# Kernel optimization log

Measured on AMD Instinct MI355X. Metric: run time of the kernel, lower is better.

## Reference

```python
import jax, jax.numpy as jnp
import numpy as np

INPUT_DIM = 80
ENC_DIM = 256
ATTN_DIM = 128
GRU_DIM = 256
B = 32
T_ENC = 800
T_DEC = 400


def setup_inputs() -> dict:
    key = jax.random.key(0)
    ks = jax.random.split(key, 12)
    s = 0.05
    d = {}
    d['enc_feat'] = jax.random.normal(ks[0], (B, T_ENC, ENC_DIM), jnp.float32)
    d['ground_truth'] = jax.random.normal(ks[1], (B, T_DEC, INPUT_DIM), jnp.float32)
    # GRU (PyTorch layout): weight_ih (3*G, in), weight_hh (3*G, G)
    d['W_ih'] = jax.random.normal(ks[2], (3 * GRU_DIM, INPUT_DIM + ENC_DIM), jnp.float32) * s
    d['W_hh'] = jax.random.normal(ks[3], (3 * GRU_DIM, GRU_DIM), jnp.float32) * s
    d['b_ih'] = jax.random.normal(ks[4], (3 * GRU_DIM,), jnp.float32) * s
    d['b_hh'] = jax.random.normal(ks[5], (3 * GRU_DIM,), jnp.float32) * s
    # Additive attention: v^T tanh(W_enc e + W_dec h + b)
    d['W_enc'] = jax.random.normal(ks[6], (ATTN_DIM, ENC_DIM), jnp.float32) * s
    d['W_dec'] = jax.random.normal(ks[7], (ATTN_DIM, GRU_DIM), jnp.float32) * s
    d['b_attn'] = jax.random.normal(ks[8], (ATTN_DIM,), jnp.float32) * s
    d['v_attn'] = jax.random.normal(ks[9], (ATTN_DIM,), jnp.float32) * s
    # output_trans: Linear(gru_dim + enc_feat_dim -> input_dim)
    d['W_out'] = jax.random.normal(ks[10], (INPUT_DIM, GRU_DIM + ENC_DIM), jnp.float32) * s
    d['b_out'] = jax.random.normal(ks[11], (INPUT_DIM,), jnp.float32) * s
    return d


def reference(enc_feat, ground_truth, W_ih, W_hh, b_ih, b_hh,
              W_enc, W_dec, b_attn, v_attn, W_out, b_out):
    # Teacher-forced decode (teacher_force_rate=1.0): max_step = T_dec,
    # input at each step is ground_truth[:, t, :].
    Bsz, T_enc, E = enc_feat.shape
    G = W_hh.shape[1]
    # Encoder projection for additive attention (step-invariant)
    enc_proj = jnp.einsum('bte,ae->bta', enc_feat, W_enc)  # (B, T_enc, attn_dim)

    def step(carry, x_t):
        h, ctx = carry  # h: (B,G), ctx: (B,E)
        inp = jnp.concatenate([x_t, ctx], axis=-1)  # (B, input_dim+E)
        gi = inp @ W_ih.T + b_ih
        gh = h @ W_hh.T + b_hh
        ir, iz, inn = jnp.split(gi, 3, axis=-1)
        hr, hz, hn = jnp.split(gh, 3, axis=-1)
        r = jax.nn.sigmoid(ir + hr)
        z = jax.nn.sigmoid(iz + hz)
        n = jnp.tanh(inn + r * hn)
        h_new = (1.0 - z) * n + z * h  # PyTorch GRU update
        # additive attention over encoder timesteps
        dec_proj = h_new @ W_dec.T + b_attn  # (B, attn_dim)
        scores = jnp.einsum('bta,a->bt', jnp.tanh(enc_proj + dec_proj[:, None, :]), v_attn)
        attn = jax.nn.softmax(scores, axis=-1)  # (B, T_enc)
        ctx_new = jnp.einsum('bt,bte->be', attn, enc_feat)  # (B, E)
        concat = jnp.concatenate([h_new, ctx_new], axis=-1)
        pred = jax.nn.log_softmax(concat @ W_out.T + b_out, axis=-1)
        return (h_new, ctx_new), (pred, attn)

    h0 = jnp.zeros((Bsz, G), enc_feat.dtype)
    c0 = jnp.zeros((Bsz, E), enc_feat.dtype)
    xs = jnp.swapaxes(ground_truth, 0, 1)  # (T_dec, B, input_dim)
    _, (preds, attns) = jax.lax.scan(step, (h0, c0), xs)
    pred_seq = jnp.swapaxes(preds, 0, 1)    # (B, T_dec, input_dim)
    attn_record = jnp.swapaxes(attns, 0, 1)  # (B, T_dec, T_enc)
    return pred_seq, attn_record
```

## Files before the change

### kernel.cpp

```cpp
#include <hip/hip_runtime.h>

#define BB    32
#define TDEC  400
#define TENC  800
#define EDIM  256
#define GDIM  256
#define ADIM  128
#define IDIM  80
#define G3    768
#define NSL   8
#define SLH   32
#define SLT   100
#define XCST  257
#define EPST  136
#define ETST  102

typedef unsigned short u16;
typedef unsigned int u32;
typedef unsigned long long u64;

__device__ __forceinline__ float b2f(u16 u) {
  union { u32 i; float f; } x; x.i = ((u32)u) << 16; return x.f;
}
__device__ __forceinline__ u16 f2b(float f) {
  union { float f; u32 u; } x; x.f = f;
  u32 u = x.u; u += 0x7fffu + ((u >> 16) & 1u);
  return (u16)(u >> 16);
}
__device__ __forceinline__ void ld8(const u16* p, float* w) {
  const uint4 q = *reinterpret_cast<const uint4*>(p);
  union { u32 i; float f; } c;
  c.i = q.x << 16;          w[0] = c.f;
  c.i = q.x & 0xffff0000u;  w[1] = c.f;
  c.i = q.y << 16;          w[2] = c.f;
  c.i = q.y & 0xffff0000u;  w[3] = c.f;
  c.i = q.z << 16;          w[4] = c.f;
  c.i = q.z & 0xffff0000u;  w[5] = c.f;
  c.i = q.w << 16;          w[6] = c.f;
  c.i = q.w & 0xffff0000u;  w[7] = c.f;
}
__device__ __forceinline__ void ldf8(const float* p, float* w) {
  const float4 a = *reinterpret_cast<const float4*>(p);
  const float4 b = *reinterpret_cast<const float4*>(p + 4);
  w[0] = a.x; w[1] = a.y; w[2] = a.z; w[3] = a.w;
  w[4] = b.x; w[5] = b.y; w[6] = b.z; w[7] = b.w;
}
__device__ __forceinline__ float fsigmoid(float x) {
  return __builtin_amdgcn_rcpf(1.f + __expf(-x));
}
__device__ __forceinline__ float ftanh(float x) {
  float e = __expf(2.f * x);
  return 1.f - 2.f * __builtin_amdgcn_rcpf(e + 1.f);
}
__device__ __forceinline__ void pst(float2* p, float v, u32 tag) {
  union { u64 u; u32 w[2]; } pk;
  pk.w[0] = __float_as_uint(v); pk.w[1] = tag;
  __hip_atomic_store((u64*)p, pk.u, __ATOMIC_RELAXED, __HIP_MEMORY_SCOPE_AGENT);
}
__device__ __forceinline__ u64 pld(const float2* p) {
  return __hip_atomic_load((const u64*)p, __ATOMIC_RELAXED,
                           __HIP_MEMORY_SCOPE_AGENT);
}
__device__ __forceinline__ float poll1(const float2* p, u32 tag) {
  for (;;) {
    const u64 x = pld(p);
    if ((u32)(x >> 32) == tag) return __uint_as_float((u32)x);
    __builtin_amdgcn_s_sleep(1);
  }
}
__device__ __forceinline__ float gather8(const float2* base, int stride,
                                         u32 tag, float init) {
  u64 x[8];
  for (;;) {
    bool ok = true;
    #pragma unroll
    for (int k = 0; k < 8; ++k) x[k] = pld(base + (size_t)k * stride);
    #pragma unroll
    for (int k = 0; k < 8; ++k) ok &= ((u32)(x[k] >> 32) == tag);
    if (ok) break;
    __builtin_amdgcn_s_sleep(1);
  }
  float s = init;
  #pragma unroll
  for (int k = 0; k < 8; ++k) s += __uint_as_float((u32)x[k]);
  return s;
}

__global__ __launch_bounds__(256) void k_gix(
    const float* __restrict__ gt, const float* __restrict__ W_ih,
    const float* __restrict__ b_ih, u16* __restrict__ gi_x) {
  __shared__ float sc_x[8][IDIM];
  const int tid = threadIdx.x;
  const int b = blockIdx.x / 50;
  const int t0 = (blockIdx.x % 50) * 8;
  for (int idx = tid; idx < 8 * IDIM; idx += 256) {
    int row = idx / IDIM, col = idx % IDIM;
    sc_x[row][col] = gt[((size_t)b * TDEC + t0 + row) * IDIM + col];
  }
  __syncthreads();
  for (int kk = 0; kk < 3; ++kk) {
    const int g = tid + 256 * kk;
    const float* wrow = W_ih + (size_t)g * 336;
    float acc[8] = {0,0,0,0,0,0,0,0};
    #pragma unroll 2
    for (int k8 = 0; k8 < IDIM / 8; ++k8) {
      float w[8]; ldf8(wrow + (k8 << 3), w);
      #pragma unroll
      for (int tt = 0; tt < 8; ++tt) {
        const float* x = &sc_x[tt][k8 << 3];
        acc[tt] += w[0]*x[0] + w[1]*x[1] + w[2]*x[2] + w[3]*x[3]
                 + w[4]*x[4] + w[5]*x[5] + w[6]*x[6] + w[7]*x[7];
      }
    }
    const float bias = b_ih[g];
    #pragma unroll
    for (int tt = 0; tt < 8; ++tt)
      gi_x[((size_t)b * TDEC + t0 + tt) * G3 + g] = f2b(acc[tt] + bias);
  }
}

__global__ __launch_bounds__(256) void k_encp(
    const float* __restrict__ enc_feat, const float* __restrict__ W_enc,
    u16* __restrict__ encp, u16* __restrict__ enc_bf) {
  __shared__ float sc_x[16][EDIM];
  const int tid = threadIdx.x;
  const int b = blockIdx.x / 50;
  const int te0 = (blockIdx.x % 50) * 16;
  for (int idx = tid; idx < 16 * EDIM; idx += 256) {
    int row = idx >> 8, col = idx & 255;
    sc_x[row][col] = enc_feat[((size_t)b * TENC + te0 + row) * EDIM + col];
  }
  __syncthreads();
  const int a = tid & 127;
  const int tg = tid >> 7;
  const float* wrow = W_enc + (size_t)a * EDIM;
  float acc[8] = {0,0,0,0,0,0,0,0};
  #pragma unroll 4
  for (int k8 = 0; k8 < EDIM / 8; ++k8) {
    float w[8]; ldf8(wrow + (k8 << 3), w);
    #pragma unroll
    for (int tt = 0; tt < 8; ++tt) {
      const float* x = &sc_x[tg * 8 + tt][k8 << 3];
      acc[tt] += w[0]*x[0] + w[1]*x[1] + w[2]*x[2] + w[3]*x[3]
               + w[4]*x[4] + w[5]*x[5] + w[6]*x[6] + w[7]*x[7];
    }
  }
  #pragma unroll
  for (int tt = 0; tt < 8; ++tt)
    encp[((size_t)b * TENC + te0 + tg * 8 + tt) * ADIM + a] = f2b(acc[tt]);
  for (int idx = tid; idx < 16 * EDIM; idx += 256)
    enc_bf[((size_t)b * TENC + te0) * EDIM + idx] = f2b(sc_x[idx >> 8][idx & 255]);
}

__global__ __launch_bounds__(512, 1) void k_decode(
    const float* __restrict__ W_ih, const float* __restrict__ W_hh,
    const float* __restrict__ b_hh, const float* __restrict__ W_dec,
    const float* __restrict__ b_attn, const float* __restrict__ v_attn,
    const u16* __restrict__ gi_x, const u16* __restrict__ encp,
    const u16* __restrict__ enc_bf, float* __restrict__ stash,
    float2* __restrict__ XhS, float2* __restrict__ DaccS,
    float2* __restrict__ XctxS, float* __restrict__ out_attn) {
  extern __shared__ __align__(16) u16 dynlds[];
  u16* encp_lds = dynlds;
  u16* enc_t    = dynlds + SLT * EPST;

  __shared__ u32 sWdp[ADIM * 17];
  __shared__ __align__(16) float sc_h[256];
  __shared__ float sc_ing[4][68];
  __shared__ float sc_inh[4][68];
  __shared__ float sc_dec[ADIM];
  __shared__ float sc_g0[96];
  __shared__ float sc_g1[96];
  __shared__ float sc_w[104];
  __shared__ float sc_v[ADIM];
  __shared__ float sc_ba[ADIM];
  __shared__ float sc_bhh[96];
  __shared__ float sc_gx[96];
  __shared__ float sc_S;

  const int tid = threadIdx.x;
  const int b = blockIdx.x & 31;
  const int j = blockIdx.x >> 5;
  const int lane = tid & 63;

  u32 wctx[32], whh[32];
  #pragma unroll
  for (int i = 0; i < 32; ++i) { wctx[i] = 0u; whh[i] = 0u; }
  if (tid < 384) {
    const int r = tid >> 2, q = tid & 3;
    const int grow = (r >> 5) * 256 + SLH * j + (r & 31);
    const float2* s1 = reinterpret_cast<const float2*>(
        W_ih + (size_t)grow * 336 + 80 + q * 64);
    const float2* s2 = reinterpret_cast<const float2*>(
        W_hh + (size_t)grow * 256 + q * 64);
    #pragma unroll
    for (int i = 0; i < 32; ++i) {
      const float2 v1 = s1[i], v2 = s2[i];
      wctx[i] = (u32)f2b(v1.x) | ((u32)f2b(v1.y) << 16);
      whh[i]  = (u32)f2b(v2.x) | ((u32)f2b(v2.y) << 16);
    }
  }
  for (int idx = tid; idx < ADIM * 16; idx += 512) {
    const int a = idx >> 4, k2 = idx & 15;
    const float2 v = *reinterpret_cast<const float2*>(
        W_dec + (size_t)a * GDIM + SLH * j + 2 * k2);
    sWdp[a * 17 + k2] = (u32)f2b(v.x) | ((u32)f2b(v.y) << 16);
  }
  for (int idx = tid; idx < SLT * ADIM; idx += 512) {
    const int te = idx >> 7, a = idx & 127;
    encp_lds[te * EPST + a] = encp[((size_t)b * TENC + SLT * j + te) * ADIM + a];
  }
  for (int idx = tid; idx < SLT * EDIM; idx += 512) {
    const int te = idx >> 8, e = idx & 255;
    enc_t[e * ETST + te] = enc_bf[((size_t)b * TENC + SLT * j + te) * EDIM + e];
  }
  if (tid < ADIM) { sc_v[tid] = v_attn[tid]; sc_ba[tid] = b_attn[tid]; }
  if (tid < 96) {
    const int grow = (tid >> 5) * 256 + SLH * j + (tid & 31);
    const float bh = b_hh[grow];
    sc_bhh[tid] = bh;
    sc_g1[tid] = bh;
    sc_gx[tid] = b2f(gi_x[((size_t)b * TDEC + 0) * G3 + grow]);
  }
  if (tid < 256) {
    sc_h[tid] = 0.f;
    sc_ing[tid >> 6][tid & 63] = 0.f;
    sc_inh[tid >> 6][tid & 63] = 0.f;
  }
  float hprev = 0.f;
  __syncthreads();

  for (int t = 0; t < TDEC; ++t) {
    const u32 tag = (u32)(t + 1);
    if (tid < 384) {
      const float* act = &sc_ing[tid & 3][0];
      float acc = 0.f;
      #pragma unroll
      for (int i = 0; i < 32; ++i) {
        union { u32 u; float f; } lo, hi;
        lo.u = wctx[i] << 16; hi.u = wctx[i] & 0xffff0000u;
        acc += lo.f * act[2 * i] + hi.f * act[2 * i + 1];
      }
      acc += __shfl_xor(acc, 1);
      acc += __shfl_xor(acc, 2);
      if ((tid & 3) == 0) sc_g0[tid >> 2] = acc + sc_gx[tid >> 2];
    }
    __syncthreads();
    if (tid < 64) {
      float hval = 0.f;
      if (lane < SLH) {
        const float gr = sc_g0[lane] + sc_g1[lane];
        const float gz = sc_g0[SLH + lane] + sc_g1[SLH + lane];
        const float rr = fsigmoid(gr);
        const float zz = fsigmoid(gz);
        const float nn = ftanh(sc_g0[2 * SLH + lane] + rr * sc_g1[2 * SLH + lane]);
        hval = (1.f - zz) * nn + zz * hprev;
        hprev = hval;
        pst(&XhS[b * GDIM + SLH * j + lane], hval, tag);
      }
      float hn[32];
      #pragma unroll
      for (int k = 0; k < 32; ++k) hn[k] = __shfl(hval, k);
      #pragma unroll
      for (int r2 = 0; r2 < 2; ++r2) {
        const int a = lane + 64 * r2;
        const u32* wp = &sWdp[a * 17];
        float acc = 0.f;
        #pragma unroll
        for (int k2 = 0; k2 < 16; ++k2) {
          const u32 w2 = wp[k2];
          union { u32 u; float f; } lo, hi;
          lo.u = w2 << 16; hi.u = w2 & 0xffff0000u;
          acc += lo.f * hn[2 * k2] + hi.f * hn[2 * k2 + 1];
        }
        pst(&DaccS[(b * NSL + j) * ADIM + a], acc, tag);
      }
    }
    if (tid < 128) {
      sc_dec[tid] = gather8(&DaccS[b * NSL * ADIM + tid], ADIM, tag, sc_ba[tid]);
    } else if (tid < 384) {
      const int g = tid - 128;
      const float hv = poll1(&XhS[b * GDIM + g], tag);
      sc_h[g] = hv;
      sc_inh[g >> 6][g & 63] = hv;
    }
    __syncthreads();
    if (tid < 400) {
      const int te = tid >> 2, q4 = tid & 3;
      const u16* ep = &encp_lds[te * EPST + q4 * 32];
      const float* dp = sc_dec + q4 * 32;
      const float* vp = sc_v + q4 * 32;
      float s = 0.f;
      #pragma unroll
      for (int k8 = 0; k8 < 4; ++k8) {
        float w[8]; ld8(ep + (k8 << 3), w);
        #pragma unroll
        for (int i = 0; i < 8; ++i) {
          const int a = (k8 << 3) + i;
          s += ftanh(w[i] + dp[a]) * vp[a];
        }
      }
      s += __shfl_xor(s, 1);
      s += __shfl_xor(s, 2);
      if (q4 == 0) sc_w[te] = __expf(s);
    } else if (tid < 448) {
      if (j == 0) {
        for (int g = tid - 400; g < 256; g += 48)
          stash[((size_t)b * TDEC + t) * 512 + g] = sc_h[g];
      }
    } else {
      const int tn = (t + 1 < TDEC) ? t + 1 : t;
      const int gl = tid - 448;
      {
        const int grow = (gl >> 5) * 256 + SLH * j + (gl & 31);
        sc_gx[gl] = b2f(gi_x[((size_t)b * TDEC + tn) * G3 + grow]);
      }
      if (gl < 32) {
        const int g2 = gl + 64;
        const int grow = (g2 >> 5) * 256 + SLH * j + (g2 & 31);
        sc_gx[g2] = b2f(gi_x[((size_t)b * TDEC + tn) * G3 + grow]);
      }
    }
    __syncthreads();
    if (tid < 256) {
      const u32* et = reinterpret_cast<const u32*>(&enc_t[tid * ETST]);
      float pc = 0.f;
      #pragma unroll
      for (int k2 = 0; k2 < 50; ++k2) {
        const u32 w2 = et[k2];
        union { u32 u; float f; } lo, hi;
        lo.u = w2 << 16; hi.u = w2 & 0xffff0000u;
        pc += sc_w[2 * k2] * lo.f + sc_w[2 * k2 + 1] * hi.f;
      }
      pst(&XctxS[(b * NSL + j) * XCST + tid], pc, tag);
    }
    if (tid < 64) {
      float v = (lane < 50) ? sc_w[lane] + sc_w[lane + 50] : 0.f;
      #pragma unroll
      for (int off = 1; off < 64; off <<= 1) v += __shfl_xor(v, off);
      if (lane == 0) pst(&XctxS[(b * NSL + j) * XCST + 256], v, tag);
    }
    if (tid < 384) {
      const float* act = &sc_inh[tid & 3][0];
      float acc = 0.f;
      #pragma unroll
      for (int i = 0; i < 32; ++i) {
        union { u32 u; float f; } lo, hi;
        lo.u = whh[i] << 16; hi.u = whh[i] & 0xffff0000u;
        acc += lo.f * act[2 * i] + hi.f * act[2 * i + 1];
      }
      acc += __shfl_xor(acc, 1);
      acc += __shfl_xor(acc, 2);
      if ((tid & 3) == 0) sc_g1[tid >> 2] = acc + sc_bhh[tid >> 2];
    }
    float csum = 0.f;
    if (tid < 256) {
      csum = gather8(&XctxS[b * NSL * XCST + tid], XCST, tag, 0.f);
    } else if (tid == 256) {
      sc_S = gather8(&XctxS[b * NSL * XCST + 256], XCST, tag, 0.f);
    }
    __syncthreads();
    {
      const float invS = __builtin_amdgcn_rcpf(sc_S);
      if (tid < 256) {
        const float cv = csum * invS;
        sc_ing[tid >> 6][tid & 63] = cv;
        if (j == 0) stash[((size_t)b * TDEC + t) * 512 + 256 + tid] = cv;
      }
      if (tid < SLT)
        out_attn[((size_t)b * TDEC + t) * TENC + SLT * j + tid] =
            sc_w[tid] * invS;
    }
    __syncthreads();
  }
}

__global__ __launch_bounds__(256) void k_pred(
    const float* __restrict__ stash, const float* __restrict__ W_out,
    const float* __restrict__ b_out, float* __restrict__ out_pred) {
  __shared__ float sc_s[4][512];
  __shared__ float sc_lp[2][4][IDIM];
  __shared__ float sc_l[4][IDIM];
  __shared__ float sc_lse[4];
  const int tid = threadIdx.x;
  const int b = blockIdx.x / 100;
  const int t0 = (blockIdx.x % 100) * 4;
  for (int idx = tid; idx < 4 * 512; idx += 256)
    sc_s[idx >> 9][idx & 511] = stash[((size_t)b * TDEC + t0) * 512 + idx];
  __syncthreads();
  const int o = tid & 127, kh = tid >> 7;
  if (o < IDIM) {
    const float* wrow = W_out + (size_t)o * 512 + kh * 256;
    float acc[4] = {0,0,0,0};
    #pragma unroll 4
    for (int k8 = 0; k8 < 32; ++k8) {
      float w[8]; ldf8(wrow + (k8 << 3), w);
      #pragma unroll
      for (int tt = 0; tt < 4; ++tt) {
        const float* x = &sc_s[tt][kh * 256 + (k8 << 3)];
        acc[tt] += w[0]*x[0] + w[1]*x[1] + w[2]*x[2] + w[3]*x[3]
                 + w[4]*x[4] + w[5]*x[5] + w[6]*x[6] + w[7]*x[7];
      }
    }
    #pragma unroll
    for (int tt = 0; tt < 4; ++tt) sc_lp[kh][tt][o] = acc[tt];
  }
  __syncthreads();
  if (tid < IDIM) {
    const float bb = b_out[tid];
    #pragma unroll
    for (int tt = 0; tt < 4; ++tt)
      sc_l[tt][tid] = sc_lp[0][tt][tid] + sc_lp[1][tt][tid] + bb;
  }
  __syncthreads();
  {
    const int w = tid >> 6, lane = tid & 63;
    const float a0 = sc_l[w][lane];
    const float a1 = (lane < IDIM - 64) ? sc_l[w][lane + 64] : -1e30f;
    float m = fmaxf(a0, a1);
    #pragma unroll
    for (int off = 1; off < 64; off <<= 1) m = fmaxf(m, __shfl_xor(m, off));
    float e = __expf(a0 - m) + ((lane < IDIM - 64) ? __expf(a1 - m) : 0.f);
    #pragma unroll
    for (int off = 1; off < 64; off <<= 1) e += __shfl_xor(e, off);
    if (lane == 0) sc_lse[w] = m + __logf(e);
  }
  __syncthreads();
  for (int idx = tid; idx < 4 * IDIM; idx += 256) {
    const int tt = idx / IDIM, oo = idx % IDIM;
    out_pred[((size_t)b * TDEC + t0 + tt) * IDIM + oo] =
        sc_l[tt][oo] - sc_lse[tt];
  }
}

extern "C" void kernel_launch(void* const* d_in, const int* in_sizes, int n_in,
                              void* d_out, int out_size, void* d_ws, size_t ws_size,
                              hipStream_t stream) {
  const float* enc_feat = (const float*)d_in[0];
  const float* gt       = (const float*)d_in[1];
  const float* W_ih     = (const float*)d_in[2];
  const float* W_hh     = (const float*)d_in[3];
  const float* b_ih     = (const float*)d_in[4];
  const float* b_hh     = (const float*)d_in[5];
  const float* W_enc    = (const float*)d_in[6];
  const float* W_dec    = (const float*)d_in[7];
  const float* b_attn   = (const float*)d_in[8];
  const float* v_attn   = (const float*)d_in[9];
  const float* W_out    = (const float*)d_in[10];
  const float* b_out    = (const float*)d_in[11];
  float* out_pred = (float*)d_out;
  float* out_attn = out_pred + (size_t)BB * TDEC * IDIM;

  char* ws = (char*)d_ws;
  size_t off = 0;
  u16* gi_x   = (u16*)(ws + off);   off += (size_t)BB * TDEC * G3 * 2;
  u16* encp   = (u16*)(ws + off);   off += (size_t)BB * TENC * ADIM * 2;
  u16* enc_bf = (u16*)(ws + off);   off += (size_t)BB * TENC * EDIM * 2;
  float* stash= (float*)(ws + off); off += (size_t)BB * TDEC * 512 * 4;
  char* zbase = ws + off;
  float2* XhS   = (float2*)(ws + off); off += (size_t)BB * GDIM * 8;
  float2* DaccS = (float2*)(ws + off); off += (size_t)BB * NSL * ADIM * 8;
  float2* XctxS = (float2*)(ws + off); off += (size_t)BB * NSL * XCST * 8;
  const size_t zbytes = (size_t)(ws + off - zbase);

  const int DYNB = (SLT * EPST + EDIM * ETST) * 2;
  static bool s_attr = false;
  if (!s_attr) {
    (void)hipFuncSetAttribute(reinterpret_cast<const void*>(k_decode),
                              hipFuncAttributeMaxDynamicSharedMemorySize, DYNB);
    s_attr = true;
  }

  hipMemsetAsync(zbase, 0, zbytes, stream);

  hipLaunchKernelGGL(k_gix, dim3(BB * 50), dim3(256), 0, stream,
                     gt, W_ih, b_ih, gi_x);
  hipLaunchKernelGGL(k_encp, dim3(BB * 50), dim3(256), 0, stream,
                     enc_feat, W_enc, encp, enc_bf);
  hipLaunchKernelGGL(k_decode, dim3(BB * NSL), dim3(512), DYNB, stream,
                     W_ih, W_hh, b_hh, W_dec, b_attn, v_attn,
                     gi_x, encp, enc_bf, stash, XhS, DaccS, XctxS, out_attn);
  hipLaunchKernelGGL(k_pred, dim3(BB * 100), dim3(256), 0, stream,
                     stash, W_out, b_out, out_pred);
}
```

Baseline: 2.831 ms.

## Replace per-element tagged polling with per-wave sentinel flags for cross-block exchange

```diff
diff --git a/kernel.cpp b/kernel.cpp
--- a/kernel.cpp
+++ b/kernel.cpp
@@ -17,7 +17,6 @@
 
 typedef unsigned short u16;
 typedef unsigned int u32;
-typedef unsigned long long u64;
 
 __device__ __forceinline__ float b2f(u16 u) {
   union { u32 i; float f; } x; x.i = ((u32)u) << 16; return x.f;
@@ -52,38 +51,17 @@
   float e = __expf(2.f * x);
   return 1.f - 2.f * __builtin_amdgcn_rcpf(e + 1.f);
 }
-__device__ __forceinline__ void pst(float2* p, float v, u32 tag) {
-  union { u64 u; u32 w[2]; } pk;
-  pk.w[0] = __float_as_uint(v); pk.w[1] = tag;
-  __hip_atomic_store((u64*)p, pk.u, __ATOMIC_RELAXED, __HIP_MEMORY_SCOPE_AGENT);
-}
-__device__ __forceinline__ u64 pld(const float2* p) {
-  return __hip_atomic_load((const u64*)p, __ATOMIC_RELAXED,
-                           __HIP_MEMORY_SCOPE_AGENT);
-}
-__device__ __forceinline__ float poll1(const float2* p, u32 tag) {
-  for (;;) {
-    const u64 x = pld(p);
-    if ((u32)(x >> 32) == tag) return __uint_as_float((u32)x);
-    __builtin_amdgcn_s_sleep(1);
-  }
-}
-__device__ __forceinline__ float gather8(const float2* base, int stride,
-                                         u32 tag, float init) {
-  u64 x[8];
-  for (;;) {
-    bool ok = true;
-    #pragma unroll
-    for (int k = 0; k < 8; ++k) x[k] = pld(base + (size_t)k * stride);
-    #pragma unroll
-    for (int k = 0; k < 8; ++k) ok &= ((u32)(x[k] >> 32) == tag);
-    if (ok) break;
-    __builtin_amdgcn_s_sleep(1);
-  }
-  float s = init;
-  #pragma unroll
-  for (int k = 0; k < 8; ++k) s += __uint_as_float((u32)x[k]);
-  return s;
+__device__ __forceinline__ void ast(float* p, float v) {
+  __hip_atomic_store(p, v, __ATOMIC_RELAXED, __HIP_MEMORY_SCOPE_AGENT);
+}
+__device__ __forceinline__ float ald(const float* p) {
+  return __hip_atomic_load(p, __ATOMIC_RELAXED, __HIP_MEMORY_SCOPE_AGENT);
+}
+__device__ __forceinline__ void asti(int* p, int v) {
+  __hip_atomic_store(p, v, __ATOMIC_RELAXED, __HIP_MEMORY_SCOPE_AGENT);
+}
+__device__ __forceinline__ int aldi(const int* p) {
+  return __hip_atomic_load(p, __ATOMIC_RELAXED, __HIP_MEMORY_SCOPE_AGENT);
 }
 
 __global__ __launch_bounds__(256) void k_gix(
@@ -158,8 +136,9 @@
     const float* __restrict__ b_attn, const float* __restrict__ v_attn,
     const u16* __restrict__ gi_x, const u16* __restrict__ encp,
     const u16* __restrict__ enc_bf, float* __restrict__ stash,
-    float2* __restrict__ XhS, float2* __restrict__ DaccS,
-    float2* __restrict__ XctxS, float* __restrict__ out_attn) {
+    float* __restrict__ Xh, float* __restrict__ Dacc,
+    float* __restrict__ Xcp, int* __restrict__ sentA,
+    int* __restrict__ sentB, float* __restrict__ out_attn) {
   extern __shared__ __align__(16) u16 dynlds[];
   u16* encp_lds = dynlds;
   u16* enc_t    = dynlds + SLT * EPST;
@@ -231,7 +210,6 @@
   __syncthreads();
 
   for (int t = 0; t < TDEC; ++t) {
-    const u32 tag = (u32)(t + 1);
     if (tid < 384) {
       const float* act = &sc_ing[tid & 3][0];
       float acc = 0.f;
@@ -256,7 +234,7 @@
         const float nn = ftanh(sc_g0[2 * SLH + lane] + rr * sc_g1[2 * SLH + lane]);
         hval = (1.f - zz) * nn + zz * hprev;
         hprev = hval;
-        pst(&XhS[b * GDIM + SLH * j + lane], hval, tag);
+        ast(&Xh[b * GDIM + SLH * j + lane], hval);
       }
       float hn[32];
       #pragma unroll
@@ -273,16 +251,28 @@
           lo.u = w2 << 16; hi.u = w2 & 0xffff0000u;
           acc += lo.f * hn[2 * k2] + hi.f * hn[2 * k2 + 1];
         }
-        pst(&DaccS[(b * NSL + j) * ADIM + a], acc, tag);
-      }
-    }
-    if (tid < 128) {
-      sc_dec[tid] = gather8(&DaccS[b * NSL * ADIM + tid], ADIM, tag, sc_ba[tid]);
+        ast(&Dacc[(b * NSL + j) * ADIM + a], acc);
+      }
+      asm volatile("s_waitcnt vmcnt(0)" ::: "memory");
+      if (lane == 0) asti(&sentA[(b * NSL + j) * 16], t + 1);
+    } else if (tid < 72) {
+      const int* sp = &sentA[(b * NSL + (tid - 64)) * 16];
+      while (aldi(sp) < t + 1) __builtin_amdgcn_s_sleep(1);
+    }
+    __syncthreads();
+    if (tid < 256) {
+      const float hv = ald(&Xh[b * GDIM + tid]);
+      sc_h[tid] = hv;
+      sc_inh[tid >> 6][tid & 63] = hv;
     } else if (tid < 384) {
-      const int g = tid - 128;
-      const float hv = poll1(&XhS[b * GDIM + g], tag);
-      sc_h[g] = hv;
-      sc_inh[g >> 6][g & 63] = hv;
+      const int a = tid - 256;
+      float x[8];
+      #pragma unroll
+      for (int k = 0; k < 8; ++k) x[k] = ald(&Dacc[(b * NSL + k) * ADIM + a]);
+      float s = sc_ba[a];
+      #pragma unroll
+      for (int k = 0; k < 8; ++k) s += x[k];
+      sc_dec[a] = s;
     }
     __syncthreads();
     if (tid < 400) {
@@ -332,13 +322,13 @@
         lo.u = w2 << 16; hi.u = w2 & 0xffff0000u;
         pc += sc_w[2 * k2] * lo.f + sc_w[2 * k2 + 1] * hi.f;
       }
-      pst(&XctxS[(b * NSL + j) * XCST + tid], pc, tag);
+      ast(&Xcp[(b * NSL + j) * XCST + tid], pc);
     }
     if (tid < 64) {
       float v = (lane < 50) ? sc_w[lane] + sc_w[lane + 50] : 0.f;
       #pragma unroll
       for (int off = 1; off < 64; off <<= 1) v += __shfl_xor(v, off);
-      if (lane == 0) pst(&XctxS[(b * NSL + j) * XCST + 256], v, tag);
+      if (lane == 0) ast(&Xcp[(b * NSL + j) * XCST + 256], v);
     }
     if (tid < 384) {
       const float* act = &sc_inh[tid & 3][0];
@@ -353,11 +343,31 @@
       acc += __shfl_xor(acc, 2);
       if ((tid & 3) == 0) sc_g1[tid >> 2] = acc + sc_bhh[tid >> 2];
     }
+    if (tid < 256) {
+      asm volatile("s_waitcnt vmcnt(0)" ::: "memory");
+      if (lane == 0)
+        asti(&sentB[(b * NSL + j) * 64 + (tid >> 6) * 16], t + 1);
+    } else if (tid >= 448 && tid < 480) {
+      const int k = (tid - 448) >> 2;
+      const int w = (tid - 448) & 3;
+      const int* sp = &sentB[(b * NSL + k) * 64 + w * 16];
+      while (aldi(sp) < t + 1) __builtin_amdgcn_s_sleep(1);
+    }
+    __syncthreads();
     float csum = 0.f;
     if (tid < 256) {
-      csum = gather8(&XctxS[b * NSL * XCST + tid], XCST, tag, 0.f);
-    } else if (tid == 256) {
-      sc_S = gather8(&XctxS[b * NSL * XCST + 256], XCST, tag, 0.f);
+      float x[8];
+      #pragma unroll
+      for (int k = 0; k < 8; ++k)
+        x[k] = ald(&Xcp[(b * NSL + k) * XCST + tid]);
+      #pragma unroll
+      for (int k = 0; k < 8; ++k) csum += x[k];
+    } else if (tid < 264) {
+      float v = ald(&Xcp[(b * NSL + (tid - 256)) * XCST + 256]);
+      v += __shfl_xor(v, 1);
+      v += __shfl_xor(v, 2);
+      v += __shfl_xor(v, 4);
+      if (tid == 256) sc_S = v;
     }
     __syncthreads();
     {
@@ -458,9 +468,11 @@
   u16* enc_bf = (u16*)(ws + off);   off += (size_t)BB * TENC * EDIM * 2;
   float* stash= (float*)(ws + off); off += (size_t)BB * TDEC * 512 * 4;
   char* zbase = ws + off;
-  float2* XhS   = (float2*)(ws + off); off += (size_t)BB * GDIM * 8;
-  float2* DaccS = (float2*)(ws + off); off += (size_t)BB * NSL * ADIM * 8;
-  float2* XctxS = (float2*)(ws + off); off += (size_t)BB * NSL * XCST * 8;
+  float* Xh   = (float*)(ws + off); off += (size_t)BB * GDIM * 4;
+  float* Dacc = (float*)(ws + off); off += (size_t)BB * NSL * ADIM * 4;
+  float* Xcp  = (float*)(ws + off); off += (size_t)BB * NSL * XCST * 4;
+  int* sentA  = (int*)(ws + off);   off += (size_t)BB * NSL * 16 * 4;
+  int* sentB  = (int*)(ws + off);   off += (size_t)BB * NSL * 64 * 4;
   const size_t zbytes = (size_t)(ws + off - zbase);
 
   const int DYNB = (SLT * EPST + EDIM * ETST) * 2;
@@ -479,7 +491,8 @@
                      enc_feat, W_enc, encp, enc_bf);
   hipLaunchKernelGGL(k_decode, dim3(BB * NSL), dim3(512), DYNB, stream,
                      W_ih, W_hh, b_hh, W_dec, b_attn, v_attn,
-                     gi_x, encp, enc_bf, stash, XhS, DaccS, XctxS, out_attn);
+                     gi_x, encp, enc_bf, stash, Xh, Dacc, Xcp,
+                     sentA, sentB, out_attn);
   hipLaunchKernelGGL(k_pred, dim3(BB * 100), dim3(256), 0, stream,
                      stash, W_out, b_out, out_pred);
 }
```

After: 3.281 ms. 15.9% more time.

## Compute decoder attention projection redundantly per block instead of cross-block reduction

Applied to the files above, without the earlier changes.

```diff
diff --git a/kernel.cpp b/kernel.cpp
--- a/kernel.cpp
+++ b/kernel.cpp
@@ -158,13 +158,12 @@
     const float* __restrict__ b_attn, const float* __restrict__ v_attn,
     const u16* __restrict__ gi_x, const u16* __restrict__ encp,
     const u16* __restrict__ enc_bf, float* __restrict__ stash,
-    float2* __restrict__ XhS, float2* __restrict__ DaccS,
-    float2* __restrict__ XctxS, float* __restrict__ out_attn) {
+    float2* __restrict__ XhS, float2* __restrict__ XcpS,
+    float* __restrict__ out_attn) {
   extern __shared__ __align__(16) u16 dynlds[];
   u16* encp_lds = dynlds;
   u16* enc_t    = dynlds + SLT * EPST;
 
-  __shared__ u32 sWdp[ADIM * 17];
   __shared__ __align__(16) float sc_h[256];
   __shared__ float sc_ing[4][68];
   __shared__ float sc_inh[4][68];
@@ -200,11 +199,16 @@
       whh[i]  = (u32)f2b(v2.x) | ((u32)f2b(v2.y) << 16);
     }
   }
-  for (int idx = tid; idx < ADIM * 16; idx += 512) {
-    const int a = idx >> 4, k2 = idx & 15;
-    const float2 v = *reinterpret_cast<const float2*>(
-        W_dec + (size_t)a * GDIM + SLH * j + 2 * k2);
-    sWdp[a * 17 + k2] = (u32)f2b(v.x) | ((u32)f2b(v.y) << 16);
+  u32 wdec[32];
+  {
+    const int a = tid >> 2, q = tid & 3;
+    const float2* s3 = reinterpret_cast<const float2*>(
+        W_dec + (size_t)a * GDIM + q * 64);
+    #pragma unroll
+    for (int i = 0; i < 32; ++i) {
+      const float2 v = s3[i];
+      wdec[i] = (u32)f2b(v.x) | ((u32)f2b(v.y) << 16);
+    }
   }
   for (int idx = tid; idx < SLT * ADIM; idx += 512) {
     const int te = idx >> 7, a = idx & 127;
@@ -247,42 +251,41 @@
     }
     __syncthreads();
     if (tid < 64) {
-      float hval = 0.f;
       if (lane < SLH) {
         const float gr = sc_g0[lane] + sc_g1[lane];
         const float gz = sc_g0[SLH + lane] + sc_g1[SLH + lane];
         const float rr = fsigmoid(gr);
         const float zz = fsigmoid(gz);
         const float nn = ftanh(sc_g0[2 * SLH + lane] + rr * sc_g1[2 * SLH + lane]);
-        hval = (1.f - zz) * nn + zz * hprev;
+        const float hval = (1.f - zz) * nn + zz * hprev;
         hprev = hval;
         pst(&XhS[b * GDIM + SLH * j + lane], hval, tag);
       }
-      float hn[32];
-      #pragma unroll
-      for (int k = 0; k < 32; ++k) hn[k] = __shfl(hval, k);
-      #pragma unroll
-      for (int r2 = 0; r2 < 2; ++r2) {
-        const int a = lane + 64 * r2;
-        const u32* wp = &sWdp[a * 17];
-        float acc = 0.f;
-        #pragma unroll
-        for (int k2 = 0; k2 < 16; ++k2) {
-          const u32 w2 = wp[k2];
-          union { u32 u; float f; } lo, hi;
-          lo.u = w2 << 16; hi.u = w2 & 0xffff0000u;
-          acc += lo.f * hn[2 * k2] + hi.f * hn[2 * k2 + 1];
-        }
-        pst(&DaccS[(b * NSL + j) * ADIM + a], acc, tag);
-      }
-    }
-    if (tid < 128) {
-      sc_dec[tid] = gather8(&DaccS[b * NSL * ADIM + tid], ADIM, tag, sc_ba[tid]);
-    } else if (tid < 384) {
-      const int g = tid - 128;
+    } else if (tid < 320) {
+      const int g = tid - 64;
       const float hv = poll1(&XhS[b * GDIM + g], tag);
       sc_h[g] = hv;
       sc_inh[g >> 6][g & 63] = hv;
+    } else if (tid < 416) {
+      const int tn = (t + 1 < TDEC) ? t + 1 : t;
+      const int gl = tid - 320;
+      const int grow = (gl >> 5) * 256 + SLH * j + (gl & 31);
+      sc_gx[gl] = b2f(gi_x[((size_t)b * TDEC + tn) * G3 + grow]);
+    }
+    __syncthreads();
+    {
+      const int a = tid >> 2, q = tid & 3;
+      const float* hp = &sc_inh[q][0];
+      float acc = 0.f;
+      #pragma unroll
+      for (int i = 0; i < 32; ++i) {
+        union { u32 u; float f; } lo, hi;
+        lo.u = wdec[i] << 16; hi.u = wdec[i] & 0xffff0000u;
+        acc += lo.f * hp[2 * i] + hi.f * hp[2 * i + 1];
+      }
+      acc += __shfl_xor(acc, 1);
+      acc += __shfl_xor(acc, 2);
+      if (q == 0) sc_dec[a] = acc + sc_ba[a];
     }
     __syncthreads();
     if (tid < 400) {
@@ -308,18 +311,6 @@
         for (int g = tid - 400; g < 256; g += 48)
           stash[((size_t)b * TDEC + t) * 512 + g] = sc_h[g];
       }
-    } else {
-      const int tn = (t + 1 < TDEC) ? t + 1 : t;
-      const int gl = tid - 448;
-      {
-        const int grow = (gl >> 5) * 256 + SLH * j + (gl & 31);
-        sc_gx[gl] = b2f(gi_x[((size_t)b * TDEC + tn) * G3 + grow]);
-      }
-      if (gl < 32) {
-        const int g2 = gl + 64;
-        const int grow = (g2 >> 5) * 256 + SLH * j + (g2 & 31);
-        sc_gx[g2] = b2f(gi_x[((size_t)b * TDEC + tn) * G3 + grow]);
-      }
     }
     __syncthreads();
     if (tid < 256) {
@@ -332,13 +323,13 @@
         lo.u = w2 << 16; hi.u = w2 & 0xffff0000u;
         pc += sc_w[2 * k2] * lo.f + sc_w[2 * k2 + 1] * hi.f;
       }
-      pst(&XctxS[(b * NSL + j) * XCST + tid], pc, tag);
+      pst(&XcpS[(b * NSL + j) * XCST + tid], pc, tag);
     }
     if (tid < 64) {
       float v = (lane < 50) ? sc_w[lane] + sc_w[lane + 50] : 0.f;
       #pragma unroll
       for (int off = 1; off < 64; off <<= 1) v += __shfl_xor(v, off);
-      if (lane == 0) pst(&XctxS[(b * NSL + j) * XCST + 256], v, tag);
+      if (lane == 0) pst(&XcpS[(b * NSL + j) * XCST + 256], v, tag);
     }
     if (tid < 384) {
       const float* act = &sc_inh[tid & 3][0];
@@ -355,9 +346,9 @@
     }
     float csum = 0.f;
     if (tid < 256) {
-      csum = gather8(&XctxS[b * NSL * XCST + tid], XCST, tag, 0.f);
+      csum = gather8(&XcpS[b * NSL * XCST + tid], XCST, tag, 0.f);
     } else if (tid == 256) {
-      sc_S = gather8(&XctxS[b * NSL * XCST + 256], XCST, tag, 0.f);
+      sc_S = gather8(&XcpS[b * NSL * XCST + 256], XCST, tag, 0.f);
     }
     __syncthreads();
     {
@@ -459,8 +450,7 @@
   float* stash= (float*)(ws + off); off += (size_t)BB * TDEC * 512 * 4;
   char* zbase = ws + off;
   float2* XhS   = (float2*)(ws + off); off += (size_t)BB * GDIM * 8;
-  float2* DaccS = (float2*)(ws + off); off += (size_t)BB * NSL * ADIM * 8;
-  float2* XctxS = (float2*)(ws + off); off += (size_t)BB * NSL * XCST * 8;
+  float2* XcpS  = (float2*)(ws + off); off += (size_t)BB * NSL * XCST * 8;
   const size_t zbytes = (size_t)(ws + off - zbase);
 
   const int DYNB = (SLT * EPST + EDIM * ETST) * 2;
@@ -479,7 +469,7 @@
                      enc_feat, W_enc, encp, enc_bf);
   hipLaunchKernelGGL(k_decode, dim3(BB * NSL), dim3(512), DYNB, stream,
                      W_ih, W_hh, b_hh, W_dec, b_attn, v_attn,
-                     gi_x, encp, enc_bf, stash, XhS, DaccS, XctxS, out_attn);
+                     gi_x, encp, enc_bf, stash, XhS, XcpS, out_attn);
   hipLaunchKernelGGL(k_pred, dim3(BB * 100), dim3(256), 0, stream,
                      stash, W_out, b_out, out_pred);
 }
```

Result: slower. 4.489 ms (+58.6%).
